# Kernel tuning notes

Hardware: AMD Instinct MI355X
Metric: run time of the kernel (lower is better)

The kernel has to match this reference:

```python
import jax, jax.numpy as jnp
import numpy as np

H = 51

def gru_cell(x, h, w_ih, w_hh, b_ih, b_hh):
    # PyTorch GRUCell: gates ordered (r, z, n)
    gi = x @ w_ih.T + b_ih            # [B, 3H]
    gh = h @ w_hh.T + b_hh            # [B, 3H]
    i_r, i_z, i_n = jnp.split(gi, 3, axis=-1)
    h_r, h_z, h_n = jnp.split(gh, 3, axis=-1)
    r = jax.nn.sigmoid(i_r + h_r)
    z = jax.nn.sigmoid(i_z + h_z)
    n = jnp.tanh(i_n + r * h_n)
    return (1.0 - z) * n + z * h


def setup_inputs() -> dict:
    key = jax.random.key(0)
    ks = jax.random.split(key, 12)
    B, T = 2048, 1024
    s = 1.0 / np.sqrt(H)
    f32 = jnp.float32
    return {
        "input": jax.random.normal(ks[0], (B, T), dtype=f32),
        "w_ih1": jax.random.normal(ks[1], (3 * H, 1), dtype=f32) * s,
        "w_hh1": jax.random.normal(ks[2], (3 * H, H), dtype=f32) * s,
        "b_ih1": jax.random.normal(ks[3], (3 * H,), dtype=f32) * s,
        "b_hh1": jax.random.normal(ks[4], (3 * H,), dtype=f32) * s,
        "w_ih2": jax.random.normal(ks[5], (3 * H, H), dtype=f32) * s,
        "w_hh2": jax.random.normal(ks[6], (3 * H, H), dtype=f32) * s,
        "b_ih2": jax.random.normal(ks[7], (3 * H,), dtype=f32) * s,
        "b_hh2": jax.random.normal(ks[8], (3 * H,), dtype=f32) * s,
        "lin_w": jax.random.normal(ks[9], (1, H), dtype=f32) * s,
        "lin_b": jax.random.normal(ks[10], (1,), dtype=f32) * s,
        "future": 0,
    }


def reference(input, w_ih1, w_hh1, b_ih1, b_hh1, w_ih2, w_hh2, b_ih2, b_hh2, lin_w, lin_b, future):
    B, T = input.shape
    h0 = jnp.zeros((B, H), dtype=input.dtype)

    def step(carry, x_t):
        h1, h2 = carry
        h1 = gru_cell(x_t, h1, w_ih1, w_hh1, b_ih1, b_hh1)
        h2 = gru_cell(h1, h2, w_ih2, w_hh2, b_ih2, b_hh2)
        out = h2 @ lin_w.T + lin_b    # [B, 1]
        return (h1, h2), out

    xs = input.T[:, :, None]          # [T, B, 1]
    (h1, h2), outs = jax.lax.scan(step, (h0, h0), xs)  # outs: [T, B, 1]
    outputs = outs[:, :, 0].T          # [B, T]

    if future > 0:
        def fstep(carry, _):
            h1, h2, out = carry
            h1 = gru_cell(out, h1, w_ih1, w_hh1, b_ih1, b_hh1)
            h2 = gru_cell(h1, h2, w_ih2, w_hh2, b_ih2, b_hh2)
            out = h2 @ lin_w.T + lin_b
            return (h1, h2, out), out
        last = outs[-1]                # [B, 1]
        _, fouts = jax.lax.scan(fstep, (h1, h2, last), None, length=future)
        outputs = jnp.concatenate([outputs, fouts[:, :, 0].T], axis=1)
    return outputs
```

## Files before the change

kernel.cpp:

```cpp
#include <hip/hip_runtime.h>

#define HH 51
#define HP 52
#define NCH 13
#define HIST_D 64
#define HIST_W 107
#define BURST 32

typedef float float4v __attribute__((ext_vector_type(4)));

__device__ __forceinline__ float sigmoid_f(float x) {
    return 1.0f / (1.0f + __expf(-x));
}
__device__ __forceinline__ float tanh_f(float x) {
    return 1.0f - 2.0f / (__expf(2.0f * x) + 1.0f);
}

__device__ __forceinline__ float sel4(const float4v v, int k) {
    const float a = (k & 1) ? v[1] : v[0];
    const float b = (k & 1) ? v[3] : v[2];
    return (k & 2) ? b : a;
}

__global__ __launch_bounds__(256, 2)
void gru_seq_kernel(const float* __restrict__ input,
                    const float* __restrict__ w_ih1,
                    const float* __restrict__ w_hh1,
                    const float* __restrict__ b_ih1,
                    const float* __restrict__ b_hh1,
                    const float* __restrict__ w_ih2,
                    const float* __restrict__ w_hh2,
                    const float* __restrict__ b_ih2,
                    const float* __restrict__ b_hh2,
                    const float* __restrict__ lin_w,
                    const float* __restrict__ lin_b,
                    float* __restrict__ out,
                    int T)
{
    __shared__ __attribute__((aligned(16))) float h1buf[2][2][HP];
    __shared__ __attribute__((aligned(16))) float gi2buf[2][3][2][HP];
    __shared__ __attribute__((aligned(16))) float h2buf[2][2][HP];
    __shared__ __attribute__((aligned(16))) float h2hist[HIST_D][HIST_W];
    __shared__ __attribute__((aligned(16))) float lwbuf[HP];

    const int tid  = threadIdx.x;
    const int wave = tid >> 6;
    const int lane = tid & 63;
    const bool act = lane < HH;
    const int li   = act ? lane : 0;
    const long long bT0 = 2LL * blockIdx.x * T;
    const long long bT1 = bT0 + T;

    for (int s = tid; s < 2 * 2 * HP; s += 256) {
        ((float*)h1buf)[s] = 0.f;
        ((float*)h2buf)[s] = 0.f;
    }
    for (int s = tid; s < 2 * 3 * 2 * HP; s += 256) ((float*)gi2buf)[s] = 0.f;
    if (tid < HP) lwbuf[tid] = (tid < HH) ? lin_w[tid] : 0.f;

    const float* wsrc = (wave == 0) ? w_hh1 : ((wave == 1) ? w_ih2 : w_hh2);

    float4v wA[NCH], wB[NCH], wC[NCH];
    #pragma unroll
    for (int c = 0; c < NCH; ++c) {
        #pragma unroll
        for (int j = 0; j < 4; ++j) {
            const int k = 4 * c + j;
            float vA = 0.f, vB = 0.f, vC = 0.f;
            if (wave < 3 && act && k < HH) {
                vA = wsrc[(li         ) * HH + k];
                vB = wsrc[(li +    HH ) * HH + k];
                vC = wsrc[(li + 2 * HH) * HH + k];
            }
            wA[c][j] = vA; wB[c][j] = vB; wC[c][j] = vC;
        }
    }

    float sA = 0.f, sB = 0.f, sC = 0.f;
    float tA = 0.f, tB = 0.f, tC = 0.f;
    float uC = 0.f;
    if (wave == 0) {
        if (act) {
            sA = b_hh1[li]          + b_ih1[li];
            sB = b_hh1[li + HH]     + b_ih1[li + HH];
            sC = b_hh1[li + 2 * HH];
            uC = b_ih1[li + 2 * HH];
            tA = w_ih1[li]; tB = w_ih1[li + HH]; tC = w_ih1[li + 2 * HH];
        }
    } else if (wave == 1) {
        if (act) { sA = b_ih2[li]; sB = b_ih2[li + HH]; sC = b_ih2[li + 2 * HH]; }
    } else if (wave == 2) {
        if (act) { sA = b_hh2[li]; sB = b_hh2[li + HH]; sC = b_hh2[li + 2 * HH]; }
    } else {
        tB = lin_b[0];
    }

    float hr0 = 0.f, hr1 = 0.f;
    float4v xb0 = {0,0,0,0}, xb1 = {0,0,0,0}, xn0 = {0,0,0,0}, xn1 = {0,0,0,0};
    if (wave == 0) {
        xb0 = *(const float4v*)(input + bT0);
        xb1 = *(const float4v*)(input + bT1);
    }

    __syncthreads();

    for (int i = 0; i <= T + 2; ++i) {
        const int wr = i & 1;
        const int rd = (i + 1) & 1;

        if (wave == 0) {
            if (i < T) {
                if ((i & 3) == 0 && i + 4 < T) {
                    xn0 = *(const float4v*)(input + bT0 + i + 4);
                    xn1 = *(const float4v*)(input + bT1 + i + 4);
                }
                const float xc0 = sel4(xb0, i & 3);
                const float xc1 = sel4(xb1, i & 3);
                const float4v* hb0 = (const float4v*)h1buf[rd][0];
                const float4v* hb1 = (const float4v*)h1buf[rd][1];
                float4v aA0 = {sA,0.f,0.f,0.f}, aB0 = {sB,0.f,0.f,0.f}, aC0 = {sC,0.f,0.f,0.f};
                float4v aA1 = {sA,0.f,0.f,0.f}, aB1 = {sB,0.f,0.f,0.f}, aC1 = {sC,0.f,0.f,0.f};
                #pragma unroll
                for (int c = 0; c < NCH; ++c) {
                    const float4v h40 = hb0[c], h41 = hb1[c];
                    aA0 += wA[c] * h40; aB0 += wB[c] * h40; aC0 += wC[c] * h40;
                    aA1 += wA[c] * h41; aB1 += wB[c] * h41; aC1 += wC[c] * h41;
                }
                const float hA0 = (aA0[0]+aA0[1]) + (aA0[2]+aA0[3]);
                const float hB0 = (aB0[0]+aB0[1]) + (aB0[2]+aB0[3]);
                const float hC0 = (aC0[0]+aC0[1]) + (aC0[2]+aC0[3]);
                const float hA1 = (aA1[0]+aA1[1]) + (aA1[2]+aA1[3]);
                const float hB1 = (aB1[0]+aB1[1]) + (aB1[2]+aB1[3]);
                const float hC1 = (aC1[0]+aC1[1]) + (aC1[2]+aC1[3]);
                const float r0 = sigmoid_f(__fmaf_rn(xc0, tA, hA0));
                const float r1 = sigmoid_f(__fmaf_rn(xc1, tA, hA1));
                const float z0 = sigmoid_f(__fmaf_rn(xc0, tB, hB0));
                const float z1 = sigmoid_f(__fmaf_rn(xc1, tB, hB1));
                const float n0 = tanh_f(__fmaf_rn(r0, hC0, __fmaf_rn(xc0, tC, uC)));
                const float n1 = tanh_f(__fmaf_rn(r1, hC1, __fmaf_rn(xc1, tC, uC)));
                hr0 = __fmaf_rn(z0, hr0 - n0, n0);
                hr1 = __fmaf_rn(z1, hr1 - n1, n1);
                if (act) { h1buf[wr][0][li] = hr0; h1buf[wr][1][li] = hr1; }
                if ((i & 3) == 3) { xb0 = xn0; xb1 = xn1; }
            }
        } else if (wave == 1) {
            if (i >= 1 && i <= T) {
                const float4v* hb0 = (const float4v*)h1buf[rd][0];
                const float4v* hb1 = (const float4v*)h1buf[rd][1];
                float4v aA0 = {sA,0.f,0.f,0.f}, aB0 = {sB,0.f,0.f,0.f}, aC0 = {sC,0.f,0.f,0.f};
                float4v aA1 = {sA,0.f,0.f,0.f}, aB1 = {sB,0.f,0.f,0.f}, aC1 = {sC,0.f,0.f,0.f};
                #pragma unroll
                for (int c = 0; c < NCH; ++c) {
                    const float4v h40 = hb0[c], h41 = hb1[c];
                    aA0 += wA[c] * h40; aB0 += wB[c] * h40; aC0 += wC[c] * h40;
                    aA1 += wA[c] * h41; aB1 += wB[c] * h41; aC1 += wC[c] * h41;
                }
                if (act) {
                    gi2buf[wr][0][0][li] = (aA0[0]+aA0[1]) + (aA0[2]+aA0[3]);
                    gi2buf[wr][1][0][li] = (aB0[0]+aB0[1]) + (aB0[2]+aB0[3]);
                    gi2buf[wr][2][0][li] = (aC0[0]+aC0[1]) + (aC0[2]+aC0[3]);
                    gi2buf[wr][0][1][li] = (aA1[0]+aA1[1]) + (aA1[2]+aA1[3]);
                    gi2buf[wr][1][1][li] = (aB1[0]+aB1[1]) + (aB1[2]+aB1[3]);
                    gi2buf[wr][2][1][li] = (aC1[0]+aC1[1]) + (aC1[2]+aC1[3]);
                }
            }
        } else if (wave == 2) {
            if (i >= 2 && i <= T + 1) {
                const float4v* hb0 = (const float4v*)h2buf[rd][0];
                const float4v* hb1 = (const float4v*)h2buf[rd][1];
                float4v aA0 = {sA,0.f,0.f,0.f}, aB0 = {sB,0.f,0.f,0.f}, aC0 = {sC,0.f,0.f,0.f};
                float4v aA1 = {sA,0.f,0.f,0.f}, aB1 = {sB,0.f,0.f,0.f}, aC1 = {sC,0.f,0.f,0.f};
                #pragma unroll
                for (int c = 0; c < NCH; ++c) {
                    const float4v h40 = hb0[c], h41 = hb1[c];
                    aA0 += wA[c] * h40; aB0 += wB[c] * h40; aC0 += wC[c] * h40;
                    aA1 += wA[c] * h41; aB1 += wB[c] * h41; aC1 += wC[c] * h41;
                }
                const float hA0 = (aA0[0]+aA0[1]) + (aA0[2]+aA0[3]);
                const float hB0 = (aB0[0]+aB0[1]) + (aB0[2]+aB0[3]);
                const float hC0 = (aC0[0]+aC0[1]) + (aC0[2]+aC0[3]);
                const float hA1 = (aA1[0]+aA1[1]) + (aA1[2]+aA1[3]);
                const float hB1 = (aB1[0]+aB1[1]) + (aB1[2]+aB1[3]);
                const float hC1 = (aC1[0]+aC1[1]) + (aC1[2]+aC1[3]);
                const float r0 = sigmoid_f(gi2buf[rd][0][0][li] + hA0);
                const float r1 = sigmoid_f(gi2buf[rd][0][1][li] + hA1);
                const float z0 = sigmoid_f(gi2buf[rd][1][0][li] + hB0);
                const float z1 = sigmoid_f(gi2buf[rd][1][1][li] + hB1);
                const float n0 = tanh_f(__fmaf_rn(r0, hC0, gi2buf[rd][2][0][li]));
                const float n1 = tanh_f(__fmaf_rn(r1, hC1, gi2buf[rd][2][1][li]));
                hr0 = __fmaf_rn(z0, hr0 - n0, n0);
                hr1 = __fmaf_rn(z1, hr1 - n1, n1);
                const int slot = (i - 2) & (HIST_D - 1);
                if (act) {
                    h2buf[wr][0][li] = hr0; h2buf[wr][1][li] = hr1;
                    h2hist[slot][li] = hr0; h2hist[slot][53 + li] = hr1;
                }
            }
        } else {
            if (i >= BURST + 2 && ((i - 2) & (BURST - 1)) == 0) {
                const int t0 = i - 2 - BURST;
                const int e  = lane >> 5;
                const int tt = t0 + (lane & 31);
                const int col = e * 53;
                float acc = tB;
                #pragma unroll
                for (int k = 0; k < HH; ++k)
                    acc = __fmaf_rn(lwbuf[k], h2hist[tt & (HIST_D - 1)][col + k], acc);
                out[(e ? bT1 : bT0) + tt] = acc;
            }
        }
        __syncthreads();
    }
}

extern "C" void kernel_launch(void* const* d_in, const int* in_sizes, int n_in,
                              void* d_out, int out_size, void* d_ws, size_t ws_size,
                              hipStream_t stream) {
    const float* input = (const float*)d_in[0];
    const float* w_ih1 = (const float*)d_in[1];
    const float* w_hh1 = (const float*)d_in[2];
    const float* b_ih1 = (const float*)d_in[3];
    const float* b_hh1 = (const float*)d_in[4];
    const float* w_ih2 = (const float*)d_in[5];
    const float* w_hh2 = (const float*)d_in[6];
    const float* b_ih2 = (const float*)d_in[7];
    const float* b_hh2 = (const float*)d_in[8];
    const float* lin_w = (const float*)d_in[9];
    const float* lin_b = (const float*)d_in[10];

    const int B = 2048;
    const int T = in_sizes[0] / B;

    float* out = (float*)d_out;
    gru_seq_kernel<<<B / 2, 256, 0, stream>>>(input, w_ih1, w_hh1, b_ih1, b_hh1,
                                              w_ih2, w_hh2, b_ih2, b_hh2,
                                              lin_w, lin_b, out, T);
}
```

Before: 2.754 ms.

## Use fp16 packed dot products for GRU recurrent matvecs

Stores the hidden states exchanged through shared memory as fp16 and keeps the weights as packed half2 registers. The matvecs then use v_dot2 fp16 dot instructions that accumulate in fp32, which halves the number of multiply-add instructions and the LDS traffic per step on the serial critical path. The cost is lower precision in the recurrent state and weights, which may accumulate error over 1024 timesteps.

```diff
diff --git a/kernel.cpp b/kernel.cpp
--- a/kernel.cpp
+++ b/kernel.cpp
@@ -2,12 +2,15 @@
 
 #define HH 51
 #define HP 52
-#define NCH 13
+#define NH2 28
+#define NU4 7
 #define HIST_D 64
 #define HIST_W 107
 #define BURST 32
 
-typedef float float4v __attribute__((ext_vector_type(4)));
+typedef float  float4v __attribute__((ext_vector_type(4)));
+typedef unsigned int uint4v __attribute__((ext_vector_type(4)));
+typedef _Float16 half2v __attribute__((ext_vector_type(2)));
 
 __device__ __forceinline__ float sigmoid_f(float x) {
     return 1.0f / (1.0f + __expf(-x));
@@ -15,11 +18,17 @@
 __device__ __forceinline__ float tanh_f(float x) {
     return 1.0f - 2.0f / (__expf(2.0f * x) + 1.0f);
 }
-
 __device__ __forceinline__ float sel4(const float4v v, int k) {
     const float a = (k & 1) ? v[1] : v[0];
     const float b = (k & 1) ? v[3] : v[2];
     return (k & 2) ? b : a;
+}
+__device__ __forceinline__ float qdot(half2v w, half2v h, float acc) {
+#if __has_builtin(__builtin_amdgcn_fdot2)
+    return __builtin_amdgcn_fdot2(w, h, acc, false);
+#else
+    return fmaf((float)w[0], (float)h[0], fmaf((float)w[1], (float)h[1], acc));
+#endif
 }
 
 __global__ __launch_bounds__(256, 2)
@@ -37,9 +46,9 @@
                     float* __restrict__ out,
                     int T)
 {
-    __shared__ __attribute__((aligned(16))) float h1buf[2][2][HP];
+    __shared__ __attribute__((aligned(16))) unsigned int h1f16[2][2][NH2];
+    __shared__ __attribute__((aligned(16))) unsigned int h2f16[2][2][NH2];
     __shared__ __attribute__((aligned(16))) float gi2buf[2][3][2][HP];
-    __shared__ __attribute__((aligned(16))) float h2buf[2][2][HP];
     __shared__ __attribute__((aligned(16))) float h2hist[HIST_D][HIST_W];
     __shared__ __attribute__((aligned(16))) float lwbuf[HP];
 
@@ -51,29 +60,33 @@
     const long long bT0 = 2LL * blockIdx.x * T;
     const long long bT1 = bT0 + T;
 
-    for (int s = tid; s < 2 * 2 * HP; s += 256) {
-        ((float*)h1buf)[s] = 0.f;
-        ((float*)h2buf)[s] = 0.f;
+    for (int s = tid; s < 2 * 2 * NH2; s += 256) {
+        ((unsigned int*)h1f16)[s] = 0u;
+        ((unsigned int*)h2f16)[s] = 0u;
     }
     for (int s = tid; s < 2 * 3 * 2 * HP; s += 256) ((float*)gi2buf)[s] = 0.f;
     if (tid < HP) lwbuf[tid] = (tid < HH) ? lin_w[tid] : 0.f;
 
     const float* wsrc = (wave == 0) ? w_hh1 : ((wave == 1) ? w_ih2 : w_hh2);
-
-    float4v wA[NCH], wB[NCH], wC[NCH];
+    half2v wA[NH2], wB[NH2], wC[NH2];
     #pragma unroll
-    for (int c = 0; c < NCH; ++c) {
-        #pragma unroll
-        for (int j = 0; j < 4; ++j) {
-            const int k = 4 * c + j;
-            float vA = 0.f, vB = 0.f, vC = 0.f;
-            if (wave < 3 && act && k < HH) {
-                vA = wsrc[(li         ) * HH + k];
-                vB = wsrc[(li +    HH ) * HH + k];
-                vC = wsrc[(li + 2 * HH) * HH + k];
-            }
-            wA[c][j] = vA; wB[c][j] = vB; wC[c][j] = vC;
+    for (int c = 0; c < NH2; ++c) {
+        const int k0 = 2 * c, k1 = 2 * c + 1;
+        half2v a = {(_Float16)0.f, (_Float16)0.f};
+        half2v b = a, d = a;
+        if (wave < 3 && act) {
+            if (k0 < HH) {
+                a[0] = (_Float16)wsrc[(li         ) * HH + k0];
+                b[0] = (_Float16)wsrc[(li +    HH ) * HH + k0];
+                d[0] = (_Float16)wsrc[(li + 2 * HH) * HH + k0];
+            }
+            if (k1 < HH) {
+                a[1] = (_Float16)wsrc[(li         ) * HH + k1];
+                b[1] = (_Float16)wsrc[(li +    HH ) * HH + k1];
+                d[1] = (_Float16)wsrc[(li + 2 * HH) * HH + k1];
+            }
         }
+        wA[c] = a; wB[c] = b; wC[c] = d;
     }
 
     float sA = 0.f, sB = 0.f, sC = 0.f;
@@ -116,83 +129,90 @@
                 }
                 const float xc0 = sel4(xb0, i & 3);
                 const float xc1 = sel4(xb1, i & 3);
-                const float4v* hb0 = (const float4v*)h1buf[rd][0];
-                const float4v* hb1 = (const float4v*)h1buf[rd][1];
-                float4v aA0 = {sA,0.f,0.f,0.f}, aB0 = {sB,0.f,0.f,0.f}, aC0 = {sC,0.f,0.f,0.f};
-                float4v aA1 = {sA,0.f,0.f,0.f}, aB1 = {sB,0.f,0.f,0.f}, aC1 = {sC,0.f,0.f,0.f};
-                #pragma unroll
-                for (int c = 0; c < NCH; ++c) {
-                    const float4v h40 = hb0[c], h41 = hb1[c];
-                    aA0 += wA[c] * h40; aB0 += wB[c] * h40; aC0 += wC[c] * h40;
-                    aA1 += wA[c] * h41; aB1 += wB[c] * h41; aC1 += wC[c] * h41;
-                }
-                const float hA0 = (aA0[0]+aA0[1]) + (aA0[2]+aA0[3]);
-                const float hB0 = (aB0[0]+aB0[1]) + (aB0[2]+aB0[3]);
-                const float hC0 = (aC0[0]+aC0[1]) + (aC0[2]+aC0[3]);
-                const float hA1 = (aA1[0]+aA1[1]) + (aA1[2]+aA1[3]);
-                const float hB1 = (aB1[0]+aB1[1]) + (aB1[2]+aB1[3]);
-                const float hC1 = (aC1[0]+aC1[1]) + (aC1[2]+aC1[3]);
-                const float r0 = sigmoid_f(__fmaf_rn(xc0, tA, hA0));
-                const float r1 = sigmoid_f(__fmaf_rn(xc1, tA, hA1));
-                const float z0 = sigmoid_f(__fmaf_rn(xc0, tB, hB0));
-                const float z1 = sigmoid_f(__fmaf_rn(xc1, tB, hB1));
-                const float n0 = tanh_f(__fmaf_rn(r0, hC0, __fmaf_rn(xc0, tC, uC)));
-                const float n1 = tanh_f(__fmaf_rn(r1, hC1, __fmaf_rn(xc1, tC, uC)));
+                const uint4v* hb0 = (const uint4v*)h1f16[rd][0];
+                const uint4v* hb1 = (const uint4v*)h1f16[rd][1];
+                float aA0 = sA, aB0 = sB, aC0 = sC;
+                float aA1 = sA, aB1 = sB, aC1 = sC;
+                #pragma unroll
+                for (int cc = 0; cc < NU4; ++cc) {
+                    const uint4v u0 = hb0[cc], u1 = hb1[cc];
+                    #pragma unroll
+                    for (int j = 0; j < 4; ++j) {
+                        const int c = 4 * cc + j;
+                        const half2v h0 = __builtin_bit_cast(half2v, (unsigned int)u0[j]);
+                        const half2v h1 = __builtin_bit_cast(half2v, (unsigned int)u1[j]);
+                        aA0 = qdot(wA[c], h0, aA0); aB0 = qdot(wB[c], h0, aB0); aC0 = qdot(wC[c], h0, aC0);
+                        aA1 = qdot(wA[c], h1, aA1); aB1 = qdot(wB[c], h1, aB1); aC1 = qdot(wC[c], h1, aC1);
+                    }
+                }
+                const float r0 = sigmoid_f(__fmaf_rn(xc0, tA, aA0));
+                const float r1 = sigmoid_f(__fmaf_rn(xc1, tA, aA1));
+                const float z0 = sigmoid_f(__fmaf_rn(xc0, tB, aB0));
+                const float z1 = sigmoid_f(__fmaf_rn(xc1, tB, aB1));
+                const float n0 = tanh_f(__fmaf_rn(r0, aC0, __fmaf_rn(xc0, tC, uC)));
+                const float n1 = tanh_f(__fmaf_rn(r1, aC1, __fmaf_rn(xc1, tC, uC)));
                 hr0 = __fmaf_rn(z0, hr0 - n0, n0);
                 hr1 = __fmaf_rn(z1, hr1 - n1, n1);
-                if (act) { h1buf[wr][0][li] = hr0; h1buf[wr][1][li] = hr1; }
+                if (act) {
+                    ((_Float16*)h1f16[wr][0])[li] = (_Float16)hr0;
+                    ((_Float16*)h1f16[wr][1])[li] = (_Float16)hr1;
+                }
                 if ((i & 3) == 3) { xb0 = xn0; xb1 = xn1; }
             }
         } else if (wave == 1) {
             if (i >= 1 && i <= T) {
-                const float4v* hb0 = (const float4v*)h1buf[rd][0];
-                const float4v* hb1 = (const float4v*)h1buf[rd][1];
-                float4v aA0 = {sA,0.f,0.f,0.f}, aB0 = {sB,0.f,0.f,0.f}, aC0 = {sC,0.f,0.f,0.f};
-                float4v aA1 = {sA,0.f,0.f,0.f}, aB1 = {sB,0.f,0.f,0.f}, aC1 = {sC,0.f,0.f,0.f};
-                #pragma unroll
-                for (int c = 0; c < NCH; ++c) {
-                    const float4v h40 = hb0[c], h41 = hb1[c];
-                    aA0 += wA[c] * h40; aB0 += wB[c] * h40; aC0 += wC[c] * h40;
-                    aA1 += wA[c] * h41; aB1 += wB[c] * h41; aC1 += wC[c] * h41;
+                const uint4v* hb0 = (const uint4v*)h1f16[rd][0];
+                const uint4v* hb1 = (const uint4v*)h1f16[rd][1];
+                float aA0 = sA, aB0 = sB, aC0 = sC;
+                float aA1 = sA, aB1 = sB, aC1 = sC;
+                #pragma unroll
+                for (int cc = 0; cc < NU4; ++cc) {
+                    const uint4v u0 = hb0[cc], u1 = hb1[cc];
+                    #pragma unroll
+                    for (int j = 0; j < 4; ++j) {
+                        const int c = 4 * cc + j;
+                        const half2v h0 = __builtin_bit_cast(half2v, (unsigned int)u0[j]);
+                        const half2v h1 = __builtin_bit_cast(half2v, (unsigned int)u1[j]);
+                        aA0 = qdot(wA[c], h0, aA0); aB0 = qdot(wB[c], h0, aB0); aC0 = qdot(wC[c], h0, aC0);
+                        aA1 = qdot(wA[c], h1, aA1); aB1 = qdot(wB[c], h1, aB1); aC1 = qdot(wC[c], h1, aC1);
+                    }
                 }
                 if (act) {
-                    gi2buf[wr][0][0][li] = (aA0[0]+aA0[1]) + (aA0[2]+aA0[3]);
-                    gi2buf[wr][1][0][li] = (aB0[0]+aB0[1]) + (aB0[2]+aB0[3]);
-                    gi2buf[wr][2][0][li] = (aC0[0]+aC0[1]) + (aC0[2]+aC0[3]);
-                    gi2buf[wr][0][1][li] = (aA1[0]+aA1[1]) + (aA1[2]+aA1[3]);
-                    gi2buf[wr][1][1][li] = (aB1[0]+aB1[1]) + (aB1[2]+aB1[3]);
-                    gi2buf[wr][2][1][li] = (aC1[0]+aC1[1]) + (aC1[2]+aC1[3]);
+                    gi2buf[wr][0][0][li] = aA0; gi2buf[wr][0][1][li] = aA1;
+                    gi2buf[wr][1][0][li] = aB0; gi2buf[wr][1][1][li] = aB1;
+                    gi2buf[wr][2][0][li] = aC0; gi2buf[wr][2][1][li] = aC1;
                 }
             }
         } else if (wave == 2) {
             if (i >= 2 && i <= T + 1) {
-                const float4v* hb0 = (const float4v*)h2buf[rd][0];
-                const float4v* hb1 = (const float4v*)h2buf[rd][1];
-                float4v aA0 = {sA,0.f,0.f,0.f}, aB0 = {sB,0.f,0.f,0.f}, aC0 = {sC,0.f,0.f,0.f};
-                float4v aA1 = {sA,0.f,0.f,0.f}, aB1 = {sB,0.f,0.f,0.f}, aC1 = {sC,0.f,0.f,0.f};
-                #pragma unroll
-                for (int c = 0; c < NCH; ++c) {
-                    const float4v h40 = hb0[c], h41 = hb1[c];
-                    aA0 += wA[c] * h40; aB0 += wB[c] * h40; aC0 += wC[c] * h40;
-                    aA1 += wA[c] * h41; aB1 += wB[c] * h41; aC1 += wC[c] * h41;
-                }
-                const float hA0 = (aA0[0]+aA0[1]) + (aA0[2]+aA0[3]);
-                const float hB0 = (aB0[0]+aB0[1]) + (aB0[2]+aB0[3]);
-                const float hC0 = (aC0[0]+aC0[1]) + (aC0[2]+aC0[3]);
-                const float hA1 = (aA1[0]+aA1[1]) + (aA1[2]+aA1[3]);
-                const float hB1 = (aB1[0]+aB1[1]) + (aB1[2]+aB1[3]);
-                const float hC1 = (aC1[0]+aC1[1]) + (aC1[2]+aC1[3]);
-                const float r0 = sigmoid_f(gi2buf[rd][0][0][li] + hA0);
-                const float r1 = sigmoid_f(gi2buf[rd][0][1][li] + hA1);
-                const float z0 = sigmoid_f(gi2buf[rd][1][0][li] + hB0);
-                const float z1 = sigmoid_f(gi2buf[rd][1][1][li] + hB1);
-                const float n0 = tanh_f(__fmaf_rn(r0, hC0, gi2buf[rd][2][0][li]));
-                const float n1 = tanh_f(__fmaf_rn(r1, hC1, gi2buf[rd][2][1][li]));
+                const uint4v* hb0 = (const uint4v*)h2f16[rd][0];
+                const uint4v* hb1 = (const uint4v*)h2f16[rd][1];
+                float aA0 = sA, aB0 = sB, aC0 = sC;
+                float aA1 = sA, aB1 = sB, aC1 = sC;
+                #pragma unroll
+                for (int cc = 0; cc < NU4; ++cc) {
+                    const uint4v u0 = hb0[cc], u1 = hb1[cc];
+                    #pragma unroll
+                    for (int j = 0; j < 4; ++j) {
+                        const int c = 4 * cc + j;
+                        const half2v h0 = __builtin_bit_cast(half2v, (unsigned int)u0[j]);
+                        const half2v h1 = __builtin_bit_cast(half2v, (unsigned int)u1[j]);
+                        aA0 = qdot(wA[c], h0, aA0); aB0 = qdot(wB[c], h0, aB0); aC0 = qdot(wC[c], h0, aC0);
+                        aA1 = qdot(wA[c], h1, aA1); aB1 = qdot(wB[c], h1, aB1); aC1 = qdot(wC[c], h1, aC1);
+                    }
+                }
+                const float r0 = sigmoid_f(gi2buf[rd][0][0][li] + aA0);
+                const float r1 = sigmoid_f(gi2buf[rd][0][1][li] + aA1);
+                const float z0 = sigmoid_f(gi2buf[rd][1][0][li] + aB0);
+                const float z1 = sigmoid_f(gi2buf[rd][1][1][li] + aB1);
+                const float n0 = tanh_f(__fmaf_rn(r0, aC0, gi2buf[rd][2][0][li]));
+                const float n1 = tanh_f(__fmaf_rn(r1, aC1, gi2buf[rd][2][1][li]));
                 hr0 = __fmaf_rn(z0, hr0 - n0, n0);
                 hr1 = __fmaf_rn(z1, hr1 - n1, n1);
                 const int slot = (i - 2) & (HIST_D - 1);
                 if (act) {
-                    h2buf[wr][0][li] = hr0; h2buf[wr][1][li] = hr1;
+                    ((_Float16*)h2f16[wr][0])[li] = (_Float16)hr0;
+                    ((_Float16*)h2f16[wr][1])[li] = (_Float16)hr1;
                     h2hist[slot][li] = hr0; h2hist[slot][53 + li] = hr1;
                 }
             }
```

New measurement: 2.264 ms. 1.22x faster.
